# Performance work log

Measured on AMD Instinct MI355X. Metric: run time of the kernel, lower is better.

Reference implementation:

```python
import jax, jax.numpy as jnp
import numpy as np

# NOTE: SoftAttn (not shown in source) is assumed to be a channel-wise softmax over the
# kernel_size**2 attention maps, as is standard in involution/dynamic-conv designs.

def conv2d(x, w, b=None, stride=1, pad=0, dil=1):
    y = jax.lax.conv_general_dilated(
        x, w, (stride, stride), [(pad, pad), (pad, pad)],
        rhs_dilation=(dil, dil), dimension_numbers=('NCHW', 'OIHW', 'NCHW'))
    return y if b is None else y + b[None, :, None, None]

def prelu(x, a):
    return jnp.where(x >= 0, x, a * x)

def pixel_shuffle(x, r):
    b, c, h, w = x.shape
    x = x.reshape(b, c // (r * r), r, r, h, w)
    x = x.transpose(0, 1, 4, 2, 5, 3)  # b, c', h, r, w, r
    return x.reshape(b, c // (r * r), h * r, w * r)

def aflb(x, aw, ab, fw):
    # Adaptive Fine-grained Local Block: per-position attention over k^2 taps,
    # broadcast across input channels, then contracted with the conv weight.
    k = 3
    C = x.shape[1]
    att = jax.nn.softmax(conv2d(x, aw, ab, pad=1), axis=1)  # [b, k*k, H, W]
    # unfold (channel-major, spatial-minor, matching torch F.unfold)
    p = jax.lax.conv_general_dilated_patches(
        x, (k, k), (1, 1), [(1, 1), (1, 1)],
        dimension_numbers=('NCHW', 'OIHW', 'NCHW'))  # [b, C*k*k, H, W]
    b_, _, H, W = p.shape
    p = p.reshape(b_, C, k * k, H, W)
    atx = p * att[:, None]  # broadcast attention over channels
    return jnp.einsum('bcphw,ocp->bohw', atx, fw.reshape(fw.shape[0], C, k * k))

def rmrs(x, wa, ba, wb, bb, wc, bc, awA, abA, fwA, awB, abB, fwB):
    o = jnp.concatenate([
        conv2d(x, wa, ba, pad=1),
        conv2d(x, wb, bb, pad=2, dil=2),
        conv2d(x, wc, bc, pad=3, dil=3)], axis=1)
    o = aflb(o, awA, abA, fwA)
    o = aflb(o, awB, abB, fwB)
    return jax.nn.relu(o + x)


def setup_inputs() -> dict:
    key = jax.random.key(0)
    ks = iter(jax.random.split(key, 64))
    def rn(shape, s=0.05):
        return jax.random.normal(next(ks), shape, jnp.float32) * s
    a = lambda: jnp.full((1,), 0.25, jnp.float32)
    d = dict(
        ms_up=rn((2, 4, 256, 256), 1.0),
        ms_org=rn((2, 4, 64, 64), 1.0),
        pan=rn((2, 1, 256, 256), 1.0),
        w_up4=rn((64, 4, 3, 3)), b_up4=jnp.zeros(64, jnp.float32), a_up4=a(),
        w_blk53=rn((30, 5, 3, 3)), b_blk53=jnp.zeros(30, jnp.float32), a_blk53=a(),
        w_blk43=rn((30, 4, 3, 3)), b_blk43=jnp.zeros(30, jnp.float32), a_blk43=a(),
        w1a=rn((20, 60, 3, 3)), b1a=jnp.zeros(20, jnp.float32),
        w1b=rn((20, 60, 3, 3)), b1b=jnp.zeros(20, jnp.float32),
        w1c=rn((20, 60, 3, 3)), b1c=jnp.zeros(20, jnp.float32),
        aw1=rn((9, 60, 3, 3)), ab1=jnp.zeros(9, jnp.float32), fw1=rn((60, 60, 3, 3)),
        aw2=rn((9, 60, 3, 3)), ab2=jnp.zeros(9, jnp.float32), fw2=rn((60, 60, 3, 3)),
        w_blk2=rn((30, 60, 3, 3)), b_blk2=jnp.zeros(30, jnp.float32), a_blk2=a(),
        w2a=rn((10, 30, 3, 3)), b2a=jnp.zeros(10, jnp.float32),
        w2b=rn((10, 30, 3, 3)), b2b=jnp.zeros(10, jnp.float32),
        w2c=rn((10, 30, 3, 3)), b2c=jnp.zeros(10, jnp.float32),
        aw3=rn((9, 30, 3, 3)), ab3=jnp.zeros(9, jnp.float32), fw3=rn((30, 30, 3, 3)),
        aw4=rn((9, 30, 3, 3)), ab4=jnp.zeros(9, jnp.float32), fw4=rn((30, 30, 3, 3)),
        w_c6=rn((4, 30, 3, 3)), b_c6=jnp.zeros(4, jnp.float32),
    )
    return d


def reference(ms_up, ms_org, pan,
              w_up4, b_up4, a_up4,
              w_blk53, b_blk53, a_blk53,
              w_blk43, b_blk43, a_blk43,
              w1a, b1a, w1b, b1b, w1c, b1c,
              aw1, ab1, fw1, aw2, ab2, fw2,
              w_blk2, b_blk2, a_blk2,
              w2a, b2a, w2b, b2b, w2c, b2c,
              aw3, ab3, fw3, aw4, ab4, fw4,
              w_c6, b_c6):
    ms_org_up = prelu(pixel_shuffle(conv2d(ms_org, w_up4, b_up4, pad=1), 4), a_up4)
    data1 = jnp.concatenate([ms_org_up, pan], axis=1)  # [b,5,H,W]
    pan_conv = prelu(conv2d(data1, w_blk53, b_blk53, pad=1), a_blk53)
    ms_up_conv = prelu(conv2d(ms_up, w_blk43, b_blk43, pad=1), a_blk43)
    out1 = jnp.concatenate([ms_up_conv, pan_conv], axis=1)  # [b,60,H,W]
    out2 = rmrs(out1, w1a, b1a, w1b, b1b, w1c, b1c, aw1, ab1, fw1, aw2, ab2, fw2)
    out3 = prelu(conv2d(out2, w_blk2, b_blk2, pad=1), a_blk2)  # [b,30,H,W]
    out3 = rmrs(out3, w2a, b2a, w2b, b2b, w2c, b2c, aw3, ab3, fw3, aw4, ab4, fw4)
    out8 = conv2d(out3, w_c6, b_c6, pad=1)
    return out8 + ms_up
```

## Files before the change

### kernel.cpp

```cpp
#include <hip/hip_runtime.h>

typedef __attribute__((ext_vector_type(8))) short short8;
typedef __attribute__((ext_vector_type(4))) float f32x4;
typedef __attribute__((ext_vector_type(4))) int i32x4;

#define HW 65536

__device__ __forceinline__ float bf2f(unsigned short u){
    union { unsigned int i; float f; } x; x.i = ((unsigned int)u) << 16; return x.f;
}
__device__ __forceinline__ unsigned short f2bf(float f){
    union { float f; unsigned int i; } x; x.f = f;
    unsigned int r = x.i + 0x7fffu + ((x.i >> 16) & 1u);
    return (unsigned short)(r >> 16);
}
__device__ __forceinline__ unsigned int pack2(float a, float b){
    return (unsigned int)f2bf(a) | ((unsigned int)f2bf(b) << 16);
}
__device__ __forceinline__ i32x4 addrelu4(i32x4 a, i32x4 b){
    i32x4 o;
#pragma unroll
    for (int k = 0; k < 4; ++k) {
        unsigned int ua = (unsigned int)a[k], ub = (unsigned int)b[k];
        float x0 = bf2f((unsigned short)(ua & 0xffff)) + bf2f((unsigned short)(ub & 0xffff));
        float x1 = bf2f((unsigned short)(ua >> 16))    + bf2f((unsigned short)(ub >> 16));
        o[k] = (int)(((unsigned int)f2bf(fmaxf(x0, 0.f))) |
                     ((unsigned int)f2bf(fmaxf(x1, 0.f)) << 16));
    }
    return o;
}

template<int PRELU>
__global__ __launch_bounds__(256, 4) void sconv2_k(
    const unsigned short* __restrict__ inA, const unsigned short* __restrict__ wfA,
    const float* __restrict__ biasA, const float* __restrict__ alA, int coffA,
    const unsigned short* __restrict__ inB, const unsigned short* __restrict__ wfB,
    const float* __restrict__ biasB, const float* __restrict__ alB, int coffB,
    unsigned short* __restrict__ outb, int cpad)
{
    constexpr int CPIN = 32, SGR = 4, SGRP = 5, SPX = 66;
    constexpr int NSTGDW = 3 * SPX * SGRP * 4;
    constexpr int ODP = 20;
    constexpr int OUTOFF = NSTGDW;
    __shared__ __align__(16) unsigned int sm[NSTGDW + 64 * ODP];
    const int tid = threadIdx.x;
    const int lane = tid & 63, wv = tid >> 6;
    const int col = lane & 15, g = lane >> 4;
    const int bx = blockIdx.x;
    const int xcd = bx & 7, t = bx >> 3;
    const int y0 = xcd * 32 + (t & 31);
    const int x0 = ((t >> 5) & 3) * 64;
    const int which = blockIdx.z >> 1, b = blockIdx.z & 1;
    const unsigned short* in = which ? inB : inA;
    const unsigned short* wfrag = which ? wfB : wfA;
    const float* bias = which ? biasB : biasA;
    const float* alphap = which ? alB : alA;
    const int coff = which ? coffB : coffA;
    const unsigned short* inb = in + (size_t)b * HW * CPIN;

#pragma unroll
    for (int rr = 0; rr < 3; ++rr) {
        const int yy = y0 + rr - 1;
        for (int u = tid; u < SPX * SGR; u += 256) {
            const int slot = u & (SGR - 1), px = u / SGR;
            const int xx = x0 - 1 + px;
            i32x4 v = {0,0,0,0};
            if ((unsigned)yy < 256u && (unsigned)xx < 256u)
                v = *(const i32x4*)(inb + (size_t)(yy * 256 + xx) * CPIN + slot * 8);
            *(i32x4*)&sm[((rr * SPX + px) * SGRP + slot) * 4] = v;
        }
    }
    if (tid < 64) sm[OUTOFF + tid * ODP + 15] = 0;
    __syncthreads();

    const short8* wp = (const short8*)wfrag;
    f32x4 acc[2][2];
#pragma unroll
    for (int mt = 0; mt < 2; ++mt)
#pragma unroll
        for (int c = 0; c < 2; ++c) acc[mt][c] = (f32x4){0.f,0.f,0.f,0.f};
#pragma unroll
    for (int tap = 0; tap < 9; ++tap) {
        const int dy = tap / 3 - 1, dx = tap % 3 - 1;
        const int rl = dy + 1;
        short8 af[2];
#pragma unroll
        for (int mt = 0; mt < 2; ++mt)
            af[mt] = wp[(tap * 2 + mt) * 64 + lane];
        const int pl = 1 + wv * 16 + col + dx;
        const int c2 = tap & 1;
        short8 bf = *(const short8*)&sm[((rl * SPX + pl) * SGRP + g) * 4];
#pragma unroll
        for (int mt = 0; mt < 2; ++mt)
            acc[mt][c2] = __builtin_amdgcn_mfma_f32_16x16x32_bf16(af[mt], bf, acc[mt][c2], 0, 0, 0);
    }
    const float al = PRELU ? __ldg(alphap) : 0.f;
    const int px = wv * 16 + col;
#pragma unroll
    for (int mt = 0; mt < 2; ++mt) {
        const f32x4 a = acc[mt][0] + acc[mt][1];
#pragma unroll
        for (int e = 0; e < 2; ++e) {
            const int rb = mt * 16 + g * 4 + e * 2;
            if (rb < 30) {
                float v0 = a[e * 2]     + __ldg(bias + rb);
                float v1 = a[e * 2 + 1] + ((rb + 1 < 30) ? __ldg(bias + rb + 1) : 0.f);
                if (PRELU) { v0 = v0 >= 0.f ? v0 : al * v0; v1 = v1 >= 0.f ? v1 : al * v1; }
                if (rb + 1 >= 30) v1 = 0.f;
                sm[OUTOFF + px * ODP + (rb >> 1)] = pack2(v0, v1);
            }
        }
    }
    __syncthreads();
    {
        const int slot = tid & 3, opx = tid >> 2;
        i32x4 v = *(i32x4*)&sm[OUTOFF + opx * ODP + slot * 4];
        const size_t go = ((size_t)b * HW + (size_t)y0 * 256 + x0 + opx) * cpad + coff + slot * 8;
        *(i32x4*)(outb + go) = v;
    }
}

template<int PRELU>
__global__ __launch_bounds__(256, 6) void sconvp_k(
    const unsigned short* __restrict__ in,
    const unsigned short* __restrict__ wfrag,
    const float* __restrict__ bias,
    const float* __restrict__ alphap,
    unsigned short* __restrict__ outb)
{
    constexpr int KK = 2, CPIN = 64, CPAD = 32;
    constexpr int SGR = 8, SGRP = 9, SPX = 34, SROWS = 4;
    constexpr int CPP = 4, ODP = 20;
    constexpr int NSTGDW = SROWS * SPX * SGRP * 4;
    constexpr int OUTOFF = NSTGDW;
    __shared__ __align__(16) unsigned int sm[NSTGDW + 64 * ODP];

    const int tid = threadIdx.x;
    const int lane = tid & 63, wv = tid >> 6;
    const int col = lane & 15, g = lane >> 4;
    const int bx = blockIdx.x;
    const int xcd = bx & 7, t = bx >> 3;
    const int y0 = xcd * 32 + (t & 15) * 2;
    const int x0 = ((t >> 4) & 7) * 32;
    const int b = blockIdx.z;
    const unsigned short* inb = in + (size_t)b * HW * CPIN;

    for (int u = tid; u < SROWS * SPX * SGR; u += 256) {
        const int slot = u & (SGR - 1);
        const int px = (u / SGR) % SPX;
        const int row = u / (SGR * SPX);
        const int yy = y0 + row - 1, xx = x0 - 1 + px;
        i32x4 v = {0,0,0,0};
        if ((unsigned)yy < 256u && (unsigned)xx < 256u)
            v = *(const i32x4*)(inb + (size_t)(yy * 256 + xx) * CPIN + slot * 8);
        *(i32x4*)&sm[((row * SPX + px) * SGRP + slot) * 4] = v;
    }
    if (tid < 64) sm[OUTOFF + tid * ODP + 15] = 0;
    __syncthreads();

    const int r = wv >> 1, xh = wv & 1;
    const short8* wp = (const short8*)wfrag;
    f32x4 acc[2][2];
#pragma unroll
    for (int mt = 0; mt < 2; ++mt)
#pragma unroll
        for (int c = 0; c < 2; ++c) acc[mt][c] = (f32x4){0.f,0.f,0.f,0.f};
#pragma unroll
    for (int tap = 0; tap < 9; ++tap) {
        const int dy = tap / 3 - 1, dx = tap % 3 - 1;
        const int rl = r + dy + 1;
        short8 af[2][KK];
#pragma unroll
        for (int mt = 0; mt < 2; ++mt)
#pragma unroll
            for (int kk = 0; kk < KK; ++kk)
                af[mt][kk] = wp[((tap * 2 + mt) * KK + kk) * 64 + lane];
        const int pl = 1 + xh * 16 + col + dx;
#pragma unroll
        for (int kk = 0; kk < KK; ++kk) {
            short8 bf = *(const short8*)&sm[((rl * SPX + pl) * SGRP + kk * 4 + g) * 4];
#pragma unroll
            for (int mt = 0; mt < 2; ++mt)
                acc[mt][kk] = __builtin_amdgcn_mfma_f32_16x16x32_bf16(af[mt][kk], bf, acc[mt][kk], 0, 0, 0);
        }
    }
    const float al = PRELU ? __ldg(alphap) : 0.f;
    const int px = xh * 16 + col;
#pragma unroll
    for (int mt = 0; mt < 2; ++mt) {
        const f32x4 a = acc[mt][0] + acc[mt][1];
#pragma unroll
        for (int e = 0; e < 2; ++e) {
            const int rb = mt * 16 + g * 4 + e * 2;
            if (rb < 30) {
                float v0 = a[e * 2]     + __ldg(bias + rb);
                float v1 = a[e * 2 + 1] + ((rb + 1 < 30) ? __ldg(bias + rb + 1) : 0.f);
                if (PRELU) { v0 = v0 >= 0.f ? v0 : al * v0; v1 = v1 >= 0.f ? v1 : al * v1; }
                if (rb + 1 >= 30) v1 = 0.f;
                sm[OUTOFF + (r * 32 + px) * ODP + (rb >> 1)] = pack2(v0, v1);
            }
        }
    }
    __syncthreads();

    for (int u = tid; u < 64 * CPP; u += 256) {
        const int slot = u & (CPP - 1), pxr = u / CPP;
        const int rr = pxr >> 5, opx = pxr & 31;
        i32x4 v = *(i32x4*)&sm[OUTOFF + pxr * ODP + slot * 4];
        const size_t go = ((size_t)b * HW + (size_t)(y0 + rr) * 256 + x0 + opx) * CPAD + slot * 8;
        *(i32x4*)(outb + go) = v;
    }
}

template<int KK, int MR>
__global__ __launch_bounds__(384, (KK == 2 ? 5 : 8)) void trident_p(
    const unsigned short* __restrict__ in,
    const unsigned short* __restrict__ wf0, const unsigned short* __restrict__ wf1,
    const unsigned short* __restrict__ wf2,
    const float* __restrict__ b0, const float* __restrict__ b1, const float* __restrict__ b2,
    unsigned short* __restrict__ outb)
{
    constexpr int CPIN = KK * 32, CPAD = KK * 32;
    constexpr int SGR = KK * 4, SGRP = SGR + 1, SPX = 38, SROWS = 8;
    constexpr int MT_ = (KK == 2) ? 2 : 1;
    constexpr int CPP = KK * 4, ODP = (CPP + 1) * 4;
    constexpr int NSTGDW = SROWS * SPX * SGRP * 4;
    __shared__ __align__(16) unsigned int sm[NSTGDW];

    const int tid = threadIdx.x;
    const int lane = tid & 63, wv = tid >> 6;
    const int col = lane & 15, g = lane >> 4;
    const int bx = blockIdx.x;
    const int xcd = bx & 7, t = bx >> 3;
    const int y0 = xcd * 32 + (t & 15) * 2;
    const int x0 = ((t >> 4) & 7) * 32;
    const int b = blockIdx.z;
    const unsigned short* inb = in + (size_t)b * HW * CPIN;

    for (int u = tid; u < SROWS * SPX * SGR; u += 384) {
        const int slot = u & (SGR - 1);
        const int px = (u / SGR) % SPX;
        const int row = u / (SGR * SPX);
        const int yy = y0 + row - 3, xx = x0 - 3 + px;
        i32x4 v = {0,0,0,0};
        if ((unsigned)yy < 256u && (unsigned)xx < 256u)
            v = *(const i32x4*)(inb + (size_t)(yy * 256 + xx) * CPIN + slot * 8);
        *(i32x4*)&sm[((row * SPX + px) * SGRP + slot) * 4] = v;
    }
    __syncthreads();

    const int r = (wv >= 3) ? 1 : 0;
    const int dil = wv - r * 3, d = dil + 1;
    const unsigned short* wfx = (dil == 0) ? wf0 : ((dil == 1) ? wf1 : wf2);
    const float* bs = (dil == 0) ? b0 : ((dil == 1) ? b1 : b2);
    const short8* wp = (const short8*)wfx;

    f32x4 acc[MT_][2][2];
#pragma unroll
    for (int mt = 0; mt < MT_; ++mt)
#pragma unroll
        for (int nf = 0; nf < 2; ++nf)
#pragma unroll
            for (int c = 0; c < 2; ++c) acc[mt][nf][c] = (f32x4){0.f,0.f,0.f,0.f};

#pragma unroll
    for (int tap = 0; tap < 9; ++tap) {
        const int dy = tap / 3 - 1, dx = tap % 3 - 1;
        const int rl = 3 + r + dy * d;
        short8 af[MT_][KK];
#pragma unroll
        for (int mt = 0; mt < MT_; ++mt)
#pragma unroll
            for (int kk = 0; kk < KK; ++kk)
                af[mt][kk] = wp[((tap * MT_ + mt) * KK + kk) * 64 + lane];
#pragma unroll
        for (int nf = 0; nf < 2; ++nf) {
            const int pl = 3 + nf * 16 + col + dx * d;
#pragma unroll
            for (int kk = 0; kk < KK; ++kk) {
                const int c2 = (KK == 2) ? kk : (tap & 1);
                short8 bf = *(const short8*)&sm[((rl * SPX + pl) * SGRP + kk * 4 + g) * 4];
#pragma unroll
                for (int mt = 0; mt < MT_; ++mt)
                    acc[mt][nf][c2] = __builtin_amdgcn_mfma_f32_16x16x32_bf16(af[mt][kk], bf, acc[mt][nf][c2], 0, 0, 0);
            }
        }
    }
    __syncthreads();

#pragma unroll
    for (int nf = 0; nf < 2; ++nf) {
        const int px = nf * 16 + col;
        const int base = (r * 32 + px) * ODP;
#pragma unroll
        for (int mt = 0; mt < MT_; ++mt) {
            const f32x4 a = acc[mt][nf][0] + acc[mt][nf][1];
#pragma unroll
            for (int e = 0; e < 2; ++e) {
                const int rb = mt * 16 + g * 4 + e * 2;
                if (rb < MR) {
                    float v0 = a[e * 2] + __ldg(bs + rb);
                    float v1 = (rb + 1 < MR) ? a[e * 2 + 1] + __ldg(bs + rb + 1) : 0.f;
                    sm[base + ((dil * MR + rb) >> 1)] = pack2(v0, v1);
                }
            }
        }
    }
    {
        constexpr int NPAD = CPP * 4 - 3 * MR / 2;
        if (tid < 64 * NPAD) {
            const int pxr = tid / NPAD, dwp = 3 * MR / 2 + tid % NPAD;
            sm[pxr * ODP + dwp] = 0;
        }
    }
    __syncthreads();

    for (int u = tid; u < 64 * CPP; u += 384) {
        const int slot = u & (CPP - 1), pxr = u / CPP;
        const int rr = pxr >> 5, opx = pxr & 31;
        i32x4 v = *(i32x4*)&sm[pxr * ODP + slot * 4];
        const size_t go = ((size_t)b * HW + (size_t)(y0 + rr) * 256 + x0 + opx) * CPAD + slot * 8;
        *(i32x4*)(outb + go) = v;
    }
}

template<int RES>
__global__ __launch_bounds__(256, 5) void aflb2_k(
    const unsigned short* __restrict__ in,
    const unsigned short* __restrict__ awf, const float* __restrict__ ab,
    const unsigned short* __restrict__ fwf,
    const unsigned short* __restrict__ res,
    unsigned short* __restrict__ outb)
{
    constexpr int KK = 2, CPIN = 64, MTT = 4, CPAD = 64;
    constexpr int SROWS = 4, SPX = 34, SGR = 8, SGRP = 9;
    constexpr int CPP = 8, ODP = (CPP + 1) * 4;
    constexpr int NSTGDW = SROWS * SPX * SGRP * 4;
    constexpr int ATOFF = NSTGDW;
    __shared__ __align__(16) unsigned int sm[ATOFF + 2 * 32 * ODP];

    const int tid = threadIdx.x;
    const int lane = tid & 63, wv = tid >> 6;
    const int col = lane & 15, g = lane >> 4;
    const int bx = blockIdx.x;
    const int xcd = bx & 7, t = bx >> 3;
    const int y0 = xcd * 32 + (t & 15) * 2;
    const int x0 = ((t >> 4) & 7) * 32;
    const int b = blockIdx.z;
    const unsigned short* inb = in + (size_t)b * HW * CPIN;

    for (int u = tid; u < SROWS * SPX * SGR; u += 256) {
        const int slot = u & (SGR - 1);
        const int px = (u / SGR) % SPX;
        const int row = u / (SGR * SPX);
        const int yy = y0 + row - 1, xx = x0 - 1 + px;
        i32x4 v = {0,0,0,0};
        if ((unsigned)yy < 256u && (unsigned)xx < 256u)
            v = *(const i32x4*)(inb + (size_t)(yy * 256 + xx) * CPIN + slot * 8);
        *(i32x4*)&sm[((row * SPX + px) * SGRP + slot) * 4] = v;
    }
    __syncthreads();

    const short8* awp = (const short8*)awf;
    const short8* fwp = (const short8*)fwf;

    {
        const int r = wv >> 1, apx0 = (wv & 1) * 16;
        f32x4 aacc[2];
        aacc[0] = (f32x4){0.f,0.f,0.f,0.f}; aacc[1] = (f32x4){0.f,0.f,0.f,0.f};
#pragma unroll
        for (int tap = 0; tap < 9; ++tap) {
            const int dy = tap / 3 - 1, dx = tap % 3 - 1;
            const int rl = r + dy + 1;
            const int pl = 1 + apx0 + col + dx;
#pragma unroll
            for (int kk = 0; kk < KK; ++kk) {
                short8 afa = awp[(tap * KK + kk) * 64 + lane];
                short8 bf = *(const short8*)&sm[((rl * SPX + pl) * SGRP + kk * 4 + g) * 4];
                aacc[kk] = __builtin_amdgcn_mfma_f32_16x16x32_bf16(afa, bf, aacc[kk], 0, 0, 0);
            }
        }
        const f32x4 aa = aacc[0] + aacc[1];
        float v[4];
        float m = -1e30f;
#pragma unroll
        for (int rr = 0; rr < 4; ++rr) {
            const int row = g * 4 + rr;
            v[rr] = (row < 9) ? (aa[rr] + __ldg(ab + row)) : -1e30f;
            m = fmaxf(m, v[rr]);
        }
        m = fmaxf(m, __shfl_xor(m, 16));
        m = fmaxf(m, __shfl_xor(m, 32));
        float e[4]; float s = 0.f;
#pragma unroll
        for (int rr = 0; rr < 4; ++rr) { e[rr] = (g * 4 + rr < 9) ? __expf(v[rr] - m) : 0.f; s += e[rr]; }
        s += __shfl_xor(s, 16);
        s += __shfl_xor(s, 32);
        const float inv = 1.f / s;
        const int px = apx0 + col;
#pragma unroll
        for (int rr = 0; rr < 4; ++rr) {
            const int row = g * 4 + rr;
            if (row < 9) sm[ATOFF + (r * 32 + px) * 9 + row] = __float_as_uint(e[rr] * inv);
        }
    }
    __syncthreads();

    const int r = wv >> 1, mth = wv & 1;
    f32x4 acc[2][2];
#pragma unroll
    for (int mtl = 0; mtl < 2; ++mtl)
#pragma unroll
        for (int nf = 0; nf < 2; ++nf) acc[mtl][nf] = (f32x4){0.f,0.f,0.f,0.f};
#pragma unroll
    for (int tap = 0; tap < 9; ++tap) {
        const int dy = tap / 3 - 1, dx = tap % 3 - 1;
        const int rl = r + dy + 1;
        float av[2];
#pragma unroll
        for (int nf = 0; nf < 2; ++nf)
            av[nf] = __uint_as_float(sm[ATOFF + (r * 32 + nf * 16 + col) * 9 + tap]);
        short8 af[2][KK];
#pragma unroll
        for (int mtl = 0; mtl < 2; ++mtl)
#pragma unroll
            for (int kk = 0; kk < KK; ++kk)
                af[mtl][kk] = fwp[((tap * MTT + mth * 2 + mtl) * KK + kk) * 64 + lane];
#pragma unroll
        for (int nf = 0; nf < 2; ++nf) {
            const int pl = 1 + nf * 16 + col + dx;
            f32x4 p[2];
            p[0] = (f32x4){0.f,0.f,0.f,0.f}; p[1] = (f32x4){0.f,0.f,0.f,0.f};
#pragma unroll
            for (int kk = 0; kk < KK; ++kk) {
                short8 bf = *(const short8*)&sm[((rl * SPX + pl) * SGRP + kk * 4 + g) * 4];
#pragma unroll
                for (int mtl = 0; mtl < 2; ++mtl)
                    p[mtl] = __builtin_amdgcn_mfma_f32_16x16x32_bf16(af[mtl][kk], bf, p[mtl], 0, 0, 0);
            }
#pragma unroll
            for (int mtl = 0; mtl < 2; ++mtl)
#pragma unroll
                for (int rr = 0; rr < 4; ++rr)
                    acc[mtl][nf][rr] = fmaf(av[nf], p[mtl][rr], acc[mtl][nf][rr]);
        }
    }
    __syncthreads();

#pragma unroll
    for (int mtl = 0; mtl < 2; ++mtl) {
        const int mt = mth * 2 + mtl;
#pragma unroll
        for (int nf = 0; nf < 2; ++nf) {
            const int px = nf * 16 + col;
            const int base = ATOFF + (r * 32 + px) * ODP;
            const int rp = mt * 8 + g * 2;
            unsigned long long w =
                (unsigned long long)pack2(acc[mtl][nf][0], acc[mtl][nf][1]) |
                ((unsigned long long)pack2(acc[mtl][nf][2], acc[mtl][nf][3]) << 32);
            *(unsigned long long*)&sm[base + rp] = w;
        }
    }
    __syncthreads();

    for (int u = tid; u < 2 * 32 * CPP; u += 256) {
        const int slot = u & (CPP - 1), pxr = u / CPP;
        const int rr = pxr >> 5, opx = pxr & 31;
        i32x4 v = *(i32x4*)&sm[ATOFF + pxr * ODP + slot * 4];
        const size_t go = ((size_t)b * HW + (size_t)(y0 + rr) * 256 + x0 + opx) * CPAD + slot * 8;
        if (RES) v = addrelu4(v, *(const i32x4*)(res + go));
        *(i32x4*)(outb + go) = v;
    }
}

template<int KK, int RPB, int RES>
__global__ __launch_bounds__(256, 4) void aflb_p(
    const unsigned short* __restrict__ in,
    const unsigned short* __restrict__ awf, const float* __restrict__ ab,
    const unsigned short* __restrict__ fwf,
    const unsigned short* __restrict__ res,
    unsigned short* __restrict__ outb)
{
    constexpr int CPIN = KK * 32, MTT = 2 * KK, CPAD = 16 * MTT;
    constexpr int SROWS = RPB + 2, SPX = 66, SGR = KK * 4, SGRP = SGR + 1;
    constexpr int CPP = CPAD / 8, ODP = (CPP + 1) * 4;
    constexpr int NSTGDW = SROWS * SPX * SGRP * 4;
    constexpr int ATOFF = NSTGDW;
    constexpr int NATT = RPB * 64 * 9;
    constexpr int OUTOFF = ATOFF + NATT;
    __shared__ __align__(16) unsigned int sm[OUTOFF + RPB * 64 * ODP];

    const int tid = threadIdx.x;
    const int lane = tid & 63, wv = tid >> 6;
    const int col = lane & 15, g = lane >> 4;
    const int bx = blockIdx.x;
    const int xcd = bx & 7, t = bx >> 3;
    const int y0 = (RPB == 1) ? (xcd * 32 + (t & 31)) : (xcd * 32 + (t & 15) * 2);
    const int xseg = (RPB == 1) ? ((t >> 5) & 3) : ((t >> 4) & 3);
    const int x0 = xseg * 64;
    const int b = blockIdx.z;
    const unsigned short* inb = in + (size_t)b * HW * CPIN;

    for (int u = tid; u < SROWS * SPX * SGR; u += 256) {
        const int slot = u & (SGR - 1);
        const int px = (u / SGR) % SPX;
        const int row = u / (SGR * SPX);
        const int yy = y0 + row - 1, xx = x0 - 1 + px;
        i32x4 v = {0,0,0,0};
        if ((unsigned)yy < 256u && (unsigned)xx < 256u)
            v = *(const i32x4*)(inb + (size_t)(yy * 256 + xx) * CPIN + slot * 8);
        *(i32x4*)&sm[((row * SPX + px) * SGRP + slot) * 4] = v;
    }
    __syncthreads();

    const short8* awp = (const short8*)awf;
    const short8* fwp = (const short8*)fwf;

    constexpr int NF1 = (RPB == 1) ? 1 : 2;
    const int arow = (RPB == 1) ? 0 : (wv >> 1);
    const int apx0 = (RPB == 1) ? (wv * 16) : ((wv & 1) * 32);
    f32x4 aacc[NF1][2];
#pragma unroll
    for (int nf = 0; nf < NF1; ++nf)
#pragma unroll
        for (int c = 0; c < 2; ++c) aacc[nf][c] = (f32x4){0.f,0.f,0.f,0.f};
#pragma unroll
    for (int tap = 0; tap < 9; ++tap) {
        const int dy = tap / 3 - 1, dx = tap % 3 - 1;
        const int rl = arow + dy + 1;
        short8 afa[KK];
#pragma unroll
        for (int kk = 0; kk < KK; ++kk)
            afa[kk] = awp[(tap * KK + kk) * 64 + lane];
#pragma unroll
        for (int nf = 0; nf < NF1; ++nf) {
            const int pl = 1 + apx0 + nf * 16 + col + dx;
#pragma unroll
            for (int kk = 0; kk < KK; ++kk) {
                const int c2 = (KK == 2) ? kk : (tap & 1);
                short8 bf = *(const short8*)&sm[((rl * SPX + pl) * SGRP + kk * 4 + g) * 4];
                aacc[nf][c2] = __builtin_amdgcn_mfma_f32_16x16x32_bf16(afa[kk], bf, aacc[nf][c2], 0, 0, 0);
            }
        }
    }
#pragma unroll
    for (int nf = 0; nf < NF1; ++nf) {
        const f32x4 aa = aacc[nf][0] + aacc[nf][1];
        float v[4];
        float m = -1e30f;
#pragma unroll
        for (int r = 0; r < 4; ++r) {
            const int row = g * 4 + r;
            v[r] = (row < 9) ? (aa[r] + __ldg(ab + row)) : -1e30f;
            m = fmaxf(m, v[r]);
        }
        m = fmaxf(m, __shfl_xor(m, 16));
        m = fmaxf(m, __shfl_xor(m, 32));
        float e[4]; float s = 0.f;
#pragma unroll
        for (int r = 0; r < 4; ++r) { e[r] = (g * 4 + r < 9) ? __expf(v[r] - m) : 0.f; s += e[r]; }
        s += __shfl_xor(s, 16);
        s += __shfl_xor(s, 32);
        const float inv = 1.f / s;
        const int px = apx0 + nf * 16 + col;
#pragma unroll
        for (int r = 0; r < 4; ++r) {
            const int row = g * 4 + r;
            if (row < 9) sm[ATOFF + (arow * 64 + px) * 9 + row] = __float_as_uint(e[r] * inv);
        }
    }
    __syncthreads();

    const int prow = (RPB == 1) ? 0 : (wv >> 1);
    const int mth  = (RPB == 1) ? (wv >> 1) : 0;
    const int nfh  = wv & 1;
    f32x4 acc[2][2];
#pragma unroll
    for (int mtl = 0; mtl < 2; ++mtl)
#pragma unroll
        for (int nf = 0; nf < 2; ++nf) acc[mtl][nf] = (f32x4){0.f,0.f,0.f,0.f};
#pragma unroll
    for (int tap = 0; tap < 9; ++tap) {
        const int dy = tap / 3 - 1, dx = tap % 3 - 1;
        const int rl = prow + dy + 1;
        float av[2];
#pragma unroll
        for (int nf = 0; nf < 2; ++nf)
            av[nf] = __uint_as_float(sm[ATOFF + (prow * 64 + nfh * 32 + nf * 16 + col) * 9 + tap]);
        short8 af[2][KK];
#pragma unroll
        for (int mtl = 0; mtl < 2; ++mtl)
#pragma unroll
            for (int kk = 0; kk < KK; ++kk)
                af[mtl][kk] = fwp[((tap * MTT + (RPB == 1 ? mth * 2 + mtl : mtl)) * KK + kk) * 64 + lane];
#pragma unroll
        for (int nf = 0; nf < 2; ++nf) {
            const int pl = 1 + nfh * 32 + nf * 16 + col + dx;
            f32x4 p[2];
            p[0] = (f32x4){0.f,0.f,0.f,0.f}; p[1] = (f32x4){0.f,0.f,0.f,0.f};
#pragma unroll
            for (int kk = 0; kk < KK; ++kk) {
                short8 bf = *(const short8*)&sm[((rl * SPX + pl) * SGRP + kk * 4 + g) * 4];
#pragma unroll
                for (int mtl = 0; mtl < 2; ++mtl)
                    p[mtl] = __builtin_amdgcn_mfma_f32_16x16x32_bf16(af[mtl][kk], bf, p[mtl], 0, 0, 0);
            }
#pragma unroll
            for (int mtl = 0; mtl < 2; ++mtl)
#pragma unroll
                for (int r = 0; r < 4; ++r)
                    acc[mtl][nf][r] = fmaf(av[nf], p[mtl][r], acc[mtl][nf][r]);
        }
    }
    __syncthreads();

#pragma unroll
    for (int mtl = 0; mtl < 2; ++mtl) {
        const int mt = (RPB == 1) ? (mth * 2 + mtl) : mtl;
#pragma unroll
        for (int nf = 0; nf < 2; ++nf) {
            const int px = nfh * 32 + nf * 16 + col;
            const int base = OUTOFF + ((RPB == 2 ? prow * 64 : 0) + px) * ODP;
            const int rp = mt * 8 + g * 2;
            unsigned long long w =
                (unsigned long long)pack2(acc[mtl][nf][0], acc[mtl][nf][1]) |
                ((unsigned long long)pack2(acc[mtl][nf][2], acc[mtl][nf][3]) << 32);
            *(unsigned long long*)&sm[base + rp] = w;
        }
    }
    __syncthreads();

    constexpr int NOUT = RPB * 64 * CPP;
    for (int u = tid; u < NOUT; u += 256) {
        const int slot = u & (CPP - 1);
        const int px = (u / CPP) & 63;
        const int r = (RPB == 2) ? (u / (CPP * 64)) : 0;
        i32x4 v = *(i32x4*)&sm[OUTOFF + ((r * 64 + px) * ODP) + slot * 4];
        const size_t go = ((size_t)b * HW + (size_t)(y0 + r) * 256 + x0 + px) * CPAD + slot * 8;
        if (RES) v = addrelu4(v, *(const i32x4*)(res + go));
        *(i32x4*)(outb + go) = v;
    }
}

__global__ __launch_bounds__(256, 4) void final_k(
    const unsigned short* __restrict__ in,
    const unsigned short* __restrict__ wfrag,
    const float* __restrict__ bias,
    const float* __restrict__ msup, float* __restrict__ outf)
{
    constexpr int CPIN = 32, NF = 2;
    const int lane = threadIdx.x & 63, wv = threadIdx.x >> 6;
    const int col = lane & 15, g = lane >> 4;
    const int bx = blockIdx.x;
    const int xcd = bx & 7, t = bx >> 3;
    const int y = xcd * 32 + (t & 31);
    const int xh = t >> 5;
    const int b = blockIdx.z;
    const int x0 = xh * 128 + wv * 32;

    const unsigned short* inb = in + (size_t)b * HW * CPIN;
    const short8 kz = {0,0,0,0,0,0,0,0};
    const short8* wp = (const short8*)wfrag;

    f32x4 acc[NF];
#pragma unroll
    for (int nf = 0; nf < NF; ++nf) acc[nf] = (f32x4){0.f,0.f,0.f,0.f};
#pragma unroll
    for (int tap = 0; tap < 9; ++tap) {
        const int dy = tap / 3 - 1, dx = tap % 3 - 1;
        const int yy = y + dy;
        const bool yok = (unsigned)yy < 256u;
        const short8 af = wp[tap * 64 + lane];
#pragma unroll
        for (int nf = 0; nf < NF; ++nf) {
            const int xx = x0 + nf * 16 + col + dx;
            const bool ok = yok && ((unsigned)xx < 256u);
            const int pix = ok ? (yy * 256 + xx) : 0;
            short8 bf = *(const short8*)(inb + (size_t)pix * CPIN + g * 8);
            if (!ok) bf = kz;
            acc[nf] = __builtin_amdgcn_mfma_f32_16x16x32_bf16(af, bf, acc[nf], 0, 0, 0);
        }
    }
#pragma unroll
    for (int nf = 0; nf < NF; ++nf) {
        const int pix = y * 256 + x0 + nf * 16 + col;
        if (g == 0) {
#pragma unroll
            for (int r = 0; r < 4; ++r) {
                const size_t oi = ((size_t)b * 4 + r) * HW + pix;
                outf[oi] = acc[nf][r] + __ldg(bias + r) + msup[oi];
            }
        }
    }
}

struct PrepDesc { const float* src; int cout, cin, kksh, mtsh, flags, dstoff, n; };
struct PrepArgs { PrepDesc d[18]; };

__global__ __launch_bounds__(256) void prep_k(PrepArgs pa, unsigned short* __restrict__ wb)
{
    const PrepDesc d = pa.d[blockIdx.y];
    const int e = blockIdx.x * 256 + threadIdx.x;
    if (e >= d.n) return;
    const int j = e & 7;
    const int lane = (e >> 3) & 63;
    const int i512 = e >> 9;
    const int kk = i512 & ((1 << d.kksh) - 1);
    const int mt = (i512 >> d.kksh) & ((1 << d.mtsh) - 1);
    const int tap = i512 >> (d.kksh + d.mtsh);
    const int rpos = mt * 16 + (lane & 15);
    const int kpos = kk * 32 + (lane >> 4) * 8 + j;
    int o = rpos, ic = kpos;
    bool ok = true;
    if (d.flags & 2) {
        if (rpos < 30) o = rpos;
        else if (rpos >= 32 && rpos < 62) o = rpos - 2;
        else ok = false;
    }
    if (d.flags & 1) {
        if (kpos < 30) ic = kpos;
        else if (kpos >= 32 && kpos < 62) ic = kpos - 2;
        else ok = false;
    }
    float v = 0.f;
    if (ok && o < d.cout && ic < d.cin) v = d.src[(o * d.cin + ic) * 9 + tap];
    wb[d.dstoff + e] = f2bf(v);
}

template<int CIN, int COUT, int OCB, int H, int W>
__launch_bounds__(256)
__global__ void upconv_k(const float* __restrict__ in, const float* __restrict__ wgt,
                         const float* __restrict__ bias, float* __restrict__ out)
{
    constexpr int HWp = H * W;
    constexpr int NOCB = COUT / OCB;
    const int tx = threadIdx.x;
    const int lx = tx & 63, ly = tx >> 6;
    const int gx = blockIdx.x * 64 + lx;
    const int gy = blockIdx.y * 4 + ly;
    const int b = blockIdx.z / NOCB;
    const int ocb = blockIdx.z % NOCB;
    const int pixp = gy * W + gx;
    const float* inb = in + (size_t)b * CIN * HWp;

    int off[9]; float mul[9];
#pragma unroll
    for (int dy = 0; dy < 3; ++dy)
#pragma unroll
        for (int dx = 0; dx < 3; ++dx) {
            int p = dy * 3 + dx;
            int yy = gy + dy - 1, xx = gx + dx - 1;
            bool okp = ((unsigned)yy < (unsigned)H) && ((unsigned)xx < (unsigned)W);
            off[p] = okp ? (yy * W + xx) : 0;
            mul[p] = okp ? 1.f : 0.f;
        }
    float acc[OCB];
#pragma unroll
    for (int o = 0; o < OCB; ++o) acc[o] = 0.f;
    const float* wbase = wgt + (size_t)(ocb * OCB) * CIN * 9;
#pragma unroll
    for (int ic = 0; ic < CIN; ++ic) {
        const float* ip = inb + (size_t)ic * HWp;
        float tv[9];
#pragma unroll
        for (int p = 0; p < 9; ++p) tv[p] = __ldg(ip + off[p]) * mul[p];
#pragma unroll
        for (int o = 0; o < OCB; ++o) {
            const float* wq = wbase + (size_t)(o * CIN + ic) * 9;
#pragma unroll
            for (int p = 0; p < 9; ++p) acc[o] = fmaf(tv[p], wq[p], acc[o]);
        }
    }
#pragma unroll
    for (int o = 0; o < OCB; ++o)
        out[((size_t)b * COUT + ocb * OCB + o) * HWp + pixp] = acc[o] + __ldg(bias + ocb * OCB + o);
}

__global__ __launch_bounds__(256) void build_inputs(
    const float* __restrict__ tup, const float* __restrict__ pan,
    const float* __restrict__ aup, const float* __restrict__ msup,
    unsigned short* __restrict__ data1, unsigned short* __restrict__ msb)
{
    const int i = blockIdx.x * 256 + threadIdx.x;
    const int b = i >> 16, pixp = i & 65535;
    const int y = pixp >> 8, x = pixp & 255;
    unsigned short o[32];
#pragma unroll
    for (int c = 0; c < 32; ++c) o[c] = 0;
    unsigned short* dst;
    if (blockIdx.y == 0) {
        const float a = __ldg(aup);
#pragma unroll
        for (int c = 0; c < 4; ++c) {
            const int ch = c * 16 + (y & 3) * 4 + (x & 3);
            float v = tup[(((size_t)b * 64 + ch) << 12) + ((y >> 2) << 6) + (x >> 2)];
            v = (v >= 0.f) ? v : a * v;
            o[c] = f2bf(v);
        }
        o[4] = f2bf(pan[((size_t)b << 16) + pixp]);
        dst = data1;
    } else {
#pragma unroll
        for (int c = 0; c < 4; ++c)
            o[c] = f2bf(msup[(((size_t)b * 4 + c) << 16) + pixp]);
        dst = msb;
    }
    short8* dp = (short8*)(dst + (size_t)i * 32);
#pragma unroll
    for (int q = 0; q < 4; ++q) {
        short8 s;
#pragma unroll
        for (int r = 0; r < 8; ++r) s[r] = (short)o[q * 8 + r];
        dp[q] = s;
    }
}

extern "C" void kernel_launch(void* const* d_in, const int* in_sizes, int n_in,
                              void* d_out, int out_size, void* d_ws, size_t ws_size,
                              hipStream_t stream) {
    const float* ms_up  = (const float*)d_in[0];
    const float* ms_org = (const float*)d_in[1];
    const float* pan    = (const float*)d_in[2];
    const float* w_up4  = (const float*)d_in[3];
    const float* b_up4  = (const float*)d_in[4];
    const float* a_up4  = (const float*)d_in[5];
    const float* w_blk53= (const float*)d_in[6];
    const float* b_blk53= (const float*)d_in[7];
    const float* a_blk53= (const float*)d_in[8];
    const float* w_blk43= (const float*)d_in[9];
    const float* b_blk43= (const float*)d_in[10];
    const float* a_blk43= (const float*)d_in[11];
    const float* w1a=(const float*)d_in[12]; const float* b1a=(const float*)d_in[13];
    const float* w1b=(const float*)d_in[14]; const float* b1b=(const float*)d_in[15];
    const float* w1c=(const float*)d_in[16]; const float* b1c=(const float*)d_in[17];
    const float* aw1=(const float*)d_in[18]; const float* ab1=(const float*)d_in[19];
    const float* fw1=(const float*)d_in[20];
    const float* aw2=(const float*)d_in[21]; const float* ab2=(const float*)d_in[22];
    const float* fw2=(const float*)d_in[23];
    const float* w_blk2=(const float*)d_in[24]; const float* b_blk2=(const float*)d_in[25]; const float* a_blk2=(const float*)d_in[26];
    const float* w2a=(const float*)d_in[27]; const float* b2a=(const float*)d_in[28];
    const float* w2b=(const float*)d_in[29]; const float* b2b=(const float*)d_in[30];
    const float* w2c=(const float*)d_in[31]; const float* b2c=(const float*)d_in[32];
    const float* aw3=(const float*)d_in[33]; const float* ab3=(const float*)d_in[34];
    const float* fw3=(const float*)d_in[35];
    const float* aw4=(const float*)d_in[36]; const float* ab4=(const float*)d_in[37];
    const float* fw4=(const float*)d_in[38];
    const float* w_c6=(const float*)d_in[39]; const float* b_c6=(const float*)d_in[40];

    float* out = (float*)d_out;
    char* ws = (char*)d_ws;

    const size_t BIG = (size_t)2 * HW * 64 * 2;
    const size_t HALF = BIG / 2;
    unsigned short* bufA = (unsigned short*)(ws);
    unsigned short* bufB = (unsigned short*)(ws + BIG);
    unsigned short* bufC = (unsigned short*)(ws + 2 * BIG);
    unsigned short* data1 = bufC;
    float*          t_up  = (float*)(ws + 2 * BIG + HALF);
    unsigned short* msb   = bufB;
    unsigned short* bufD = bufC;
    unsigned short* bufE = bufB;
    unsigned short* bufF = bufA;
    unsigned short* wb = (unsigned short*)(ws + 3 * BIG);

    if (ws_size < 3 * BIG + 1000000) return;

    PrepArgs pa;
    int off = 0, li = 0;
    auto add = [&](const float* s, int cout, int cin, int mtsh, int kksh, int flags) {
        const int n = 9 << (mtsh + kksh + 9);
        pa.d[li].src = s; pa.d[li].cout = cout; pa.d[li].cin = cin;
        pa.d[li].kksh = kksh; pa.d[li].mtsh = mtsh; pa.d[li].flags = flags;
        pa.d[li].dstoff = off; pa.d[li].n = n;
        int ret = off; off += n; ++li; return ret;
    };
    const int o_blk43 = add(w_blk43, 30, 4, 1, 0, 0);
    const int o_blk53 = add(w_blk53, 30, 5, 1, 0, 0);
    const int o_w1a   = add(w1a, 20, 60, 1, 1, 1);
    const int o_w1b   = add(w1b, 20, 60, 1, 1, 1);
    const int o_w1c   = add(w1c, 20, 60, 1, 1, 1);
    const int o_aw1   = add(aw1,  9, 60, 0, 1, 0);
    const int o_fw1   = add(fw1, 60, 60, 2, 1, 0);
    const int o_aw2   = add(aw2,  9, 60, 0, 1, 0);
    const int o_fw2   = add(fw2, 60, 60, 2, 1, 2);
    const int o_blk2  = add(w_blk2, 30, 60, 1, 1, 1);
    const int o_w2a   = add(w2a, 10, 30, 0, 0, 0);
    const int o_w2b   = add(w2b, 10, 30, 0, 0, 0);
    const int o_w2c   = add(w2c, 10, 30, 0, 0, 0);
    const int o_aw3   = add(aw3,  9, 30, 0, 0, 0);
    const int o_fw3   = add(fw3, 30, 30, 1, 0, 0);
    const int o_aw4   = add(aw4,  9, 30, 0, 0, 0);
    const int o_fw4   = add(fw4, 30, 30, 1, 0, 0);
    const int o_c6    = add(w_c6,  4, 30, 0, 0, 0);

    prep_k<<<dim3(144, 18), 256, 0, stream>>>(pa, wb);

    upconv_k<4, 64, 16, 64, 64><<<dim3(1, 16, 8), 256, 0, stream>>>(ms_org, w_up4, b_up4, t_up);
    build_inputs<<<dim3(512, 2), 256, 0, stream>>>(t_up, pan, a_up4, ms_up, data1, msb);

    const dim3 B256(256), B384(384);
    const dim3 G2(1024, 1, 4);
    const dim3 GP(1024, 1, 2);
    const dim3 GH(512, 1, 2);

    sconv2_k<1><<<G2,B256,0,stream>>>(msb, wb+o_blk43, b_blk43, a_blk43, 0,
                                      data1, wb+o_blk53, b_blk53, a_blk53, 32,
                                      bufA, 64);

    trident_p<2,20><<<GP,B384,0,stream>>>(bufA, wb+o_w1a, wb+o_w1b, wb+o_w1c, b1a, b1b, b1c, bufB);
    aflb2_k<0><<<GP,B256,0,stream>>>(bufB, wb+o_aw1, ab1, wb+o_fw1, nullptr, bufC);
    aflb2_k<1><<<GP,B256,0,stream>>>(bufC, wb+o_aw2, ab2, wb+o_fw2, bufA,   bufB);

    sconvp_k<1><<<GP,B256,0,stream>>>(bufB, wb+o_blk2, b_blk2, a_blk2, bufD);

    trident_p<1,10><<<GP,B384,0,stream>>>(bufD, wb+o_w2a, wb+o_w2b, wb+o_w2c, b2a, b2b, b2c, bufE);
    aflb_p<1,2,0><<<GH,B256,0,stream>>>(bufE, wb+o_aw3, ab3, wb+o_fw3, nullptr, bufF);
    aflb_p<1,2,1><<<GH,B256,0,stream>>>(bufF, wb+o_aw4, ab4, wb+o_fw4, bufD,   bufE);

    final_k<<<GH,B256,0,stream>>>(bufE, wb+o_c6, b_c6, ms_up, out);
}
```

Baseline: 188.7 us.

## Enlarge trident conv tile to 4 rows and reuse weight fragments across rows

The trident dilated-conv kernel now processes a 32x4 pixel tile per block instead of 32x2, halving the grid. Each wave handles one dilation and one 16-pixel half-row across four rows, so each weight fragment load feeds four row MFMAs instead of two. The halo staging overhead per output shrinks (10 staged rows for 4 outputs instead of 8 for 2). In exchange there is more shared memory and more accumulator registers per block, and the launch-bounds occupancy hints are lowered.

```diff
diff --git a/kernel.cpp b/kernel.cpp
--- a/kernel.cpp
+++ b/kernel.cpp
@@ -213,7 +213,7 @@
 }
 
 template<int KK, int MR>
-__global__ __launch_bounds__(384, (KK == 2 ? 5 : 8)) void trident_p(
+__global__ __launch_bounds__(384, (KK == 2 ? 4 : 6)) void trident_q(
     const unsigned short* __restrict__ in,
     const unsigned short* __restrict__ wf0, const unsigned short* __restrict__ wf1,
     const unsigned short* __restrict__ wf2,
@@ -221,7 +221,7 @@
     unsigned short* __restrict__ outb)
 {
     constexpr int CPIN = KK * 32, CPAD = KK * 32;
-    constexpr int SGR = KK * 4, SGRP = SGR + 1, SPX = 38, SROWS = 8;
+    constexpr int SGR = KK * 4, SGRP = SGR + 1, SPX = 38, SROWS = 10;
     constexpr int MT_ = (KK == 2) ? 2 : 1;
     constexpr int CPP = KK * 4, ODP = (CPP + 1) * 4;
     constexpr int NSTGDW = SROWS * SPX * SGRP * 4;
@@ -232,8 +232,8 @@
     const int col = lane & 15, g = lane >> 4;
     const int bx = blockIdx.x;
     const int xcd = bx & 7, t = bx >> 3;
-    const int y0 = xcd * 32 + (t & 15) * 2;
-    const int x0 = ((t >> 4) & 7) * 32;
+    const int y0 = xcd * 32 + (t & 7) * 4;
+    const int x0 = ((t >> 3) & 7) * 32;
     const int b = blockIdx.z;
     const unsigned short* inb = in + (size_t)b * HW * CPIN;
 
@@ -249,73 +249,68 @@
     }
     __syncthreads();
 
-    const int r = (wv >= 3) ? 1 : 0;
-    const int dil = wv - r * 3, d = dil + 1;
+    const int dil = wv >> 1, d = dil + 1, xh = wv & 1;
     const unsigned short* wfx = (dil == 0) ? wf0 : ((dil == 1) ? wf1 : wf2);
     const float* bs = (dil == 0) ? b0 : ((dil == 1) ? b1 : b2);
     const short8* wp = (const short8*)wfx;
 
-    f32x4 acc[MT_][2][2];
-#pragma unroll
-    for (int mt = 0; mt < MT_; ++mt)
-#pragma unroll
-        for (int nf = 0; nf < 2; ++nf)
-#pragma unroll
-            for (int c = 0; c < 2; ++c) acc[mt][nf][c] = (f32x4){0.f,0.f,0.f,0.f};
+    f32x4 acc[4][MT_];
+#pragma unroll
+    for (int rr = 0; rr < 4; ++rr)
+#pragma unroll
+        for (int mt = 0; mt < MT_; ++mt) acc[rr][mt] = (f32x4){0.f,0.f,0.f,0.f};
 
 #pragma unroll
     for (int tap = 0; tap < 9; ++tap) {
         const int dy = tap / 3 - 1, dx = tap % 3 - 1;
-        const int rl = 3 + r + dy * d;
         short8 af[MT_][KK];
 #pragma unroll
         for (int mt = 0; mt < MT_; ++mt)
 #pragma unroll
             for (int kk = 0; kk < KK; ++kk)
                 af[mt][kk] = wp[((tap * MT_ + mt) * KK + kk) * 64 + lane];
-#pragma unroll
-        for (int nf = 0; nf < 2; ++nf) {
-            const int pl = 3 + nf * 16 + col + dx * d;
+        const int pl = 3 + xh * 16 + col + dx * d;
+#pragma unroll
+        for (int rr = 0; rr < 4; ++rr) {
+            const int rl = 3 + rr + dy * d;
 #pragma unroll
             for (int kk = 0; kk < KK; ++kk) {
-                const int c2 = (KK == 2) ? kk : (tap & 1);
                 short8 bf = *(const short8*)&sm[((rl * SPX + pl) * SGRP + kk * 4 + g) * 4];
 #pragma unroll
                 for (int mt = 0; mt < MT_; ++mt)
-                    acc[mt][nf][c2] = __builtin_amdgcn_mfma_f32_16x16x32_bf16(af[mt][kk], bf, acc[mt][nf][c2], 0, 0, 0);
+                    acc[rr][mt] = __builtin_amdgcn_mfma_f32_16x16x32_bf16(af[mt][kk], bf, acc[rr][mt], 0, 0, 0);
             }
         }
     }
     __syncthreads();
 
-#pragma unroll
-    for (int nf = 0; nf < 2; ++nf) {
-        const int px = nf * 16 + col;
-        const int base = (r * 32 + px) * ODP;
-#pragma unroll
-        for (int mt = 0; mt < MT_; ++mt) {
-            const f32x4 a = acc[mt][nf][0] + acc[mt][nf][1];
-#pragma unroll
-            for (int e = 0; e < 2; ++e) {
-                const int rb = mt * 16 + g * 4 + e * 2;
-                if (rb < MR) {
-                    float v0 = a[e * 2] + __ldg(bs + rb);
-                    float v1 = (rb + 1 < MR) ? a[e * 2 + 1] + __ldg(bs + rb + 1) : 0.f;
-                    sm[base + ((dil * MR + rb) >> 1)] = pack2(v0, v1);
+    {
+        const int px = xh * 16 + col;
+#pragma unroll
+        for (int rr = 0; rr < 4; ++rr) {
+            const int base = (rr * 32 + px) * ODP;
+#pragma unroll
+            for (int mt = 0; mt < MT_; ++mt) {
+#pragma unroll
+                for (int e = 0; e < 2; ++e) {
+                    const int rb = mt * 16 + g * 4 + e * 2;
+                    if (rb < MR) {
+                        float v0 = acc[rr][mt][e * 2] + __ldg(bs + rb);
+                        float v1 = (rb + 1 < MR) ? acc[rr][mt][e * 2 + 1] + __ldg(bs + rb + 1) : 0.f;
+                        sm[base + ((dil * MR + rb) >> 1)] = pack2(v0, v1);
+                    }
                 }
             }
         }
-    }
-    {
         constexpr int NPAD = CPP * 4 - 3 * MR / 2;
-        if (tid < 64 * NPAD) {
-            const int pxr = tid / NPAD, dwp = 3 * MR / 2 + tid % NPAD;
+        for (int u = tid; u < 128 * NPAD; u += 384) {
+            const int pxr = u / NPAD, dwp = 3 * MR / 2 + u % NPAD;
             sm[pxr * ODP + dwp] = 0;
         }
     }
     __syncthreads();
 
-    for (int u = tid; u < 64 * CPP; u += 384) {
+    for (int u = tid; u < 128 * CPP; u += 384) {
         const int slot = u & (CPP - 1), pxr = u / CPP;
         const int rr = pxr >> 5, opx = pxr & 31;
         i32x4 v = *(i32x4*)&sm[pxr * ODP + slot * 4];
@@ -901,19 +896,20 @@
     const dim3 B256(256), B384(384);
     const dim3 G2(1024, 1, 4);
     const dim3 GP(1024, 1, 2);
+    const dim3 GQ(512, 1, 2);
     const dim3 GH(512, 1, 2);
 
     sconv2_k<1><<<G2,B256,0,stream>>>(msb, wb+o_blk43, b_blk43, a_blk43, 0,
                                       data1, wb+o_blk53, b_blk53, a_blk53, 32,
                                       bufA, 64);
 
-    trident_p<2,20><<<GP,B384,0,stream>>>(bufA, wb+o_w1a, wb+o_w1b, wb+o_w1c, b1a, b1b, b1c, bufB);
+    trident_q<2,20><<<GQ,B384,0,stream>>>(bufA, wb+o_w1a, wb+o_w1b, wb+o_w1c, b1a, b1b, b1c, bufB);
     aflb2_k<0><<<GP,B256,0,stream>>>(bufB, wb+o_aw1, ab1, wb+o_fw1, nullptr, bufC);
     aflb2_k<1><<<GP,B256,0,stream>>>(bufC, wb+o_aw2, ab2, wb+o_fw2, bufA,   bufB);
 
     sconvp_k<1><<<GP,B256,0,stream>>>(bufB, wb+o_blk2, b_blk2, a_blk2, bufD);
 
-    trident_p<1,10><<<GP,B384,0,stream>>>(bufD, wb+o_w2a, wb+o_w2b, wb+o_w2c, b2a, b2b, b2c, bufE);
+    trident_q<1,10><<<GQ,B384,0,stream>>>(bufD, wb+o_w2a, wb+o_w2b, wb+o_w2c, b2a, b2b, b2c, bufE);
     aflb_p<1,2,0><<<GH,B256,0,stream>>>(bufE, wb+o_aw3, ab3, wb+o_fw3, nullptr, bufF);
     aflb_p<1,2,1><<<GH,B256,0,stream>>>(bufF, wb+o_aw4, ab4, wb+o_fw4, bufD,   bufE);
 
```

Result: no change. 190.4 us (+0.9%).
